# Performance work log

Measured on AMD Instinct MI355X. Metric: run time of the kernel, lower is better.

The kernel has to match this reference:

```python
import jax, jax.numpy as jnp
import numpy as np

DIM, INNER, NH = 256, 64, 8
HD = INNER // NH  # 8
B, H, W = 2, 48, 48
EPS = 1e-6


def _ln2d(x, w, b):
    # channel-first LayerNorm over dim=1, biased variance (matches LayerNorm2d)
    u = x.mean(axis=1, keepdims=True)
    s = ((x - u) ** 2).mean(axis=1, keepdims=True)
    xn = (x - u) / jnp.sqrt(s + EPS)
    return w[None, :, None, None] * xn + b[None, :, None, None]


def _conv1x1(x, w, b):
    return jnp.einsum('oc,bchw->bohw', w, x) + b[None, :, None, None]


def _attn(q, k, v):
    # q,k,v: [B, INNER, H, W] -> global attention over HW tokens per head
    Bq, C, Hh, Ww = q.shape
    split = lambda t: t.reshape(Bq, NH, HD, Hh * Ww)
    q, k, v = split(q), split(k), split(v)
    scale = HD ** -0.5
    attn = jnp.einsum('bhdn,bhdm->bhnm', q, k) * scale  # [B,nh,HW,HW]
    attn = jax.nn.softmax(attn, axis=-1)
    out = jnp.einsum('bhnm,bhdm->bhdn', attn, v)
    return out.reshape(Bq, C, Hh, Ww)


def setup_inputs() -> dict:
    key = jax.random.key(0)
    ks = jax.random.split(key, 12)
    w = lambda k, o, i: jax.random.normal(k, (o, i), dtype=jnp.float32) * 0.02
    d = {
        'f_rgb': jax.random.normal(ks[0], (B, DIM, H, W), dtype=jnp.float32),
        'f_ir': jax.random.normal(ks[1], (B, DIM, H, W), dtype=jnp.float32),
        'nr_w': jnp.ones(DIM), 'nr_b': jnp.zeros(DIM),
        'ni_w': jnp.ones(DIM), 'ni_b': jnp.zeros(DIM),
        'qr_w': w(ks[2], INNER, DIM), 'qr_b': jnp.zeros(INNER),
        'kvi_w': w(ks[3], 2 * INNER, DIM), 'kvi_b': jnp.zeros(2 * INNER),
        'qi_w': w(ks[4], INNER, DIM), 'qi_b': jnp.zeros(INNER),
        'kvr_w': w(ks[5], 2 * INNER, DIM), 'kvr_b': jnp.zeros(2 * INNER),
        'pr_w': w(ks[6], DIM, INNER), 'pr_b': jnp.zeros(DIM),
        'pr_lnw': jnp.ones(DIM), 'pr_lnb': jnp.zeros(DIM),
        'pi_w': w(ks[7], DIM, INNER), 'pi_b': jnp.zeros(DIM),
        'pi_lnw': jnp.ones(DIM), 'pi_lnb': jnp.zeros(DIM),
        'gr_w': w(ks[8], DIM, 2 * DIM), 'gr_b': jnp.zeros(DIM),
        'gi_w': w(ks[9], DIM, 2 * DIM), 'gi_b': jnp.zeros(DIM),
    }
    return d


def reference(f_rgb, f_ir, nr_w, nr_b, ni_w, ni_b, qr_w, qr_b, kvi_w, kvi_b,
              qi_w, qi_b, kvr_w, kvr_b, pr_w, pr_b, pr_lnw, pr_lnb,
              pi_w, pi_b, pi_lnw, pi_lnb, gr_w, gr_b, gi_w, gi_b):
    n_rgb = _ln2d(f_rgb, nr_w, nr_b)
    n_ir = _ln2d(f_ir, ni_w, ni_b)

    # RGB queries attend to IR keys/values
    q_r = _conv1x1(n_rgb, qr_w, qr_b)
    kv_i = _conv1x1(n_ir, kvi_w, kvi_b)
    k_i, v_i = kv_i[:, :INNER], kv_i[:, INNER:]
    rgb_cross = _attn(q_r, k_i, v_i)
    rgb_cross = _ln2d(_conv1x1(rgb_cross, pr_w, pr_b), pr_lnw, pr_lnb)
    gate_r = jax.nn.sigmoid(_conv1x1(jnp.concatenate([f_rgb, rgb_cross], axis=1), gr_w, gr_b))
    f_rgb_out = f_rgb + gate_r * rgb_cross

    # IR queries attend to RGB keys/values
    q_i = _conv1x1(n_ir, qi_w, qi_b)
    kv_r = _conv1x1(n_rgb, kvr_w, kvr_b)
    k_r, v_r = kv_r[:, :INNER], kv_r[:, INNER:]
    ir_cross = _attn(q_i, k_r, v_r)
    ir_cross = _ln2d(_conv1x1(ir_cross, pi_w, pi_b), pi_lnw, pi_lnb)
    gate_i = jax.nn.sigmoid(_conv1x1(jnp.concatenate([f_ir, ir_cross], axis=1), gi_w, gi_b))
    f_ir_out = f_ir + gate_i * ir_cross

    return (f_rgb_out, f_ir_out)
```

## Files before the change

kernel.cpp:

```cpp
#include <hip/hip_runtime.h>

static constexpr int kDim   = 256;
static constexpr int kInner = 64;
static constexpr int kNH    = 8;
static constexpr int kB     = 2;
static constexpr int kP     = 2304;
static constexpr float kScaleL2 = 0.5100697891920077f;
static constexpr float kEps   = 1e-6f;

typedef __fp16   fp16x2 __attribute__((ext_vector_type(2)));
typedef _Float16 half4f __attribute__((ext_vector_type(4)));
typedef _Float16 half8  __attribute__((ext_vector_type(8)));
typedef float    f32x4  __attribute__((ext_vector_type(4)));

static constexpr size_t oXq  = 0;
static constexpr size_t oQ16 = 2359296;
static constexpr size_t oK16 = 2949120;
static constexpr size_t oV16 = 3538944;
static constexpr size_t oA16 = 4128768;
static constexpr size_t oW16 = 7077888;
static constexpr size_t kInpStride = 294912;

__global__ __launch_bounds__(256) void prep(
    const float* __restrict__ x0, const float* __restrict__ w0,
    const float* __restrict__ b0, const float* __restrict__ x1,
    const float* __restrict__ w1, const float* __restrict__ b1,
    _Float16* __restrict__ Xq,
    const float* __restrict__ qr_w, const float* __restrict__ kvr_w,
    const float* __restrict__ qi_w, const float* __restrict__ kvi_w,
    const float* __restrict__ pr_w, const float* __restrict__ pi_w,
    const float* __restrict__ gr_w, const float* __restrict__ gi_w,
    _Float16* __restrict__ w16)
{
    if (blockIdx.x >= 576) {
        const int flat = blockIdx.x - 576;
        const int y = flat >> 6, x = flat & 63;
        const float* src; _Float16* dst; int n;
        _Float16* Aq = w16;
        _Float16* Ap = w16 + 98304;
        _Float16* Ag = w16 + 131072;
        switch (y) {
            case 0: src = qr_w;  dst = Aq;          n = 16384;  break;
            case 1: src = kvr_w; dst = Aq + 16384;  n = 32768;  break;
            case 2: src = qi_w;  dst = Aq + 49152;  n = 16384;  break;
            case 3: src = kvi_w; dst = Aq + 65536;  n = 32768;  break;
            case 4: src = pr_w;  dst = Ap;          n = 16384;  break;
            case 5: src = pi_w;  dst = Ap + 16384;  n = 16384;  break;
            case 6: src = gr_w;  dst = Ag;          n = 131072; break;
            default:src = gi_w;  dst = Ag + 131072; n = 131072; break;
        }
        for (int i = x * 256 + threadIdx.x; i < n; i += 64 * 256)
            dst[i] = (_Float16)src[i];
        return;
    }
    __shared__ float sb[16][16];
    __shared__ float ssb[16][16];
    const int fid = blockIdx.x;
    const int xcd = fid & 7, q = fid >> 3;
    const int inp = (xcd >> 2) & 1, bb = (xcd >> 1) & 1, half = xcd & 1;
    const float* x = inp ? x1 : x0;
    const float* w = inp ? w1 : w0;
    const float* b = inp ? b1 : b0;
    const int pos = threadIdx.x & 15;
    const int grp = threadIdx.x >> 4;
    const int p   = half * 1152 + q * 16 + pos;
    const size_t base = (size_t)bb * kDim * kP + p;
    const int c0 = grp * 16;

    float v[16];
    float s = 0.f, ss = 0.f;
    #pragma unroll
    for (int j = 0; j < 16; ++j) {
        v[j] = x[base + (size_t)(c0 + j) * kP];
        s += v[j]; ss += v[j] * v[j];
    }
    sb[grp][pos] = s; ssb[grp][pos] = ss;
    __syncthreads();
    float st = 0.f, sst = 0.f;
    #pragma unroll
    for (int g = 0; g < 16; ++g) { st += sb[g][pos]; sst += ssb[g][pos]; }
    const float mean = st * (1.f / kDim);
    const float rstd = rsqrtf(sst * (1.f / kDim) - mean * mean + kEps);
    half8 h0, h1;
    #pragma unroll
    for (int j = 0; j < 8; ++j) {
        h0[j] = (_Float16)((v[j]     - mean) * rstd * w[c0 + j]     + b[c0 + j]);
        h1[j] = (_Float16)((v[j + 8] - mean) * rstd * w[c0 + j + 8] + b[c0 + j + 8]);
    }
    _Float16* dst = Xq + ((size_t)(inp * 2 + bb) * kP + p) * 256 + c0;
    *(half8*)dst       = h0;
    *(half8*)(dst + 8) = h1;
}

template <int M, int K, int EPI>
__global__ __launch_bounds__(256) void gemm_f16(
    const _Float16* __restrict__ A,
    const _Float16* __restrict__ B,
    const float* __restrict__ b0, const float* __restrict__ b1,
    const float* __restrict__ b2, const float* __restrict__ b3,
    _Float16* __restrict__ o16a, _Float16* __restrict__ o16b, _Float16* __restrict__ o16c,
    const float* __restrict__ f0, const float* __restrict__ f1,
    float* __restrict__ outp)
{
    constexpr int MT64 = M / 64;
    const int fid = blockIdx.x;
    const int xcd = fid & 7, q = fid >> 3;
    const int s = (xcd >> 2) & 1, bb = (xcd >> 1) & 1, half = xcd & 1;
    const int ot64 = (q % MT64) * 64;
    const int pt   = q / MT64;
    const int wv = threadIdx.x >> 6, lane = threadIdx.x & 63;
    const int r16 = lane & 15, g = lane >> 4;
    const int ot = ot64 + wv * 16;
    const int p0 = half * 1152 + pt * 64;
    const int combo = s * 2 + bb;

    const _Float16* Ar = A + ((size_t)s * M + ot + r16) * K + 8 * g;
    const _Float16* Br = B + ((size_t)combo * kP + p0 + r16) * K + 8 * g;
    f32x4 acc0[4], acc1[4];
    #pragma unroll
    for (int ps = 0; ps < 4; ++ps) {
        acc0[ps] = (f32x4){0.f, 0.f, 0.f, 0.f};
        acc1[ps] = (f32x4){0.f, 0.f, 0.f, 0.f};
    }
    #pragma unroll 4
    for (int c0 = 0; c0 < K; c0 += 32) {
        const half8 a8 = *(const half8*)(Ar + c0);
        half8 b8[4];
        #pragma unroll
        for (int ps = 0; ps < 4; ++ps)
            b8[ps] = *(const half8*)(Br + (size_t)(16 * ps) * K + c0);
        const half4f al = {a8[0], a8[1], a8[2], a8[3]};
        const half4f ah = {a8[4], a8[5], a8[6], a8[7]};
        #pragma unroll
        for (int ps = 0; ps < 4; ++ps) {
            const half4f bl = {b8[ps][0], b8[ps][1], b8[ps][2], b8[ps][3]};
            const half4f bh = {b8[ps][4], b8[ps][5], b8[ps][6], b8[ps][7]};
            acc0[ps] = __builtin_amdgcn_mfma_f32_16x16x16f16(al, bl, acc0[ps], 0, 0, 0);
            acc1[ps] = __builtin_amdgcn_mfma_f32_16x16x16f16(ah, bh, acc1[ps], 0, 0, 0);
        }
    }
    const int obase = ot + 4 * g;

    #pragma unroll
    for (int ps = 0; ps < 4; ++ps) {
        float acc[4];
        #pragma unroll
        for (int i = 0; i < 4; ++i) acc[i] = acc0[ps][i] + acc1[ps][i];
        const int p = p0 + 16 * ps + r16;

        if constexpr (EPI == 0) {
            const int dlo = 4 * (g & 1);
            if (ot < 64) {
                const float* qb = s ? b1 : b0;
                const float4 bv = *(const float4*)(qb + obase);
                const int h = (ot >> 3) + (g >> 1);
                half4f o = { (_Float16)((acc[0] + bv.x) * kScaleL2), (_Float16)((acc[1] + bv.y) * kScaleL2),
                             (_Float16)((acc[2] + bv.z) * kScaleL2), (_Float16)((acc[3] + bv.w) * kScaleL2) };
                *(half4f*)(o16a + (((size_t)combo * 8 + h) * kP + p) * 8 + dlo) = o;
            } else if (ot < 128) {
                const float* kb = s ? b3 : b2;
                const float4 bv = *(const float4*)(kb + obase - 64);
                const int h = ((ot - 64) >> 3) + (g >> 1);
                half4f o = { (_Float16)(acc[0] + bv.x), (_Float16)(acc[1] + bv.y),
                             (_Float16)(acc[2] + bv.z), (_Float16)(acc[3] + bv.w) };
                *(half4f*)(o16b + (((size_t)combo * 8 + h) * kP + p) * 8 + dlo) = o;
            } else {
                const float* kb = s ? b3 : b2;
                const float4 bv = *(const float4*)(kb + obase - 64);
                const int h = ((ot - 128) >> 3) + (g >> 1);
                const float* bvp = (const float*)&bv;
                #pragma unroll
                for (int i = 0; i < 4; ++i)
                    o16c[(((size_t)combo * 8 + h) * 8 + dlo + i) * kP + p] = (_Float16)(acc[i] + bvp[i]);
            }
        } else {
            const float* gb = s ? b1 : b0;
            const float4 bv = *(const float4*)(gb + obase);
            const float* bvp = (const float*)&bv;
            const half4f cx = *(const half4f*)(B + ((size_t)combo * kP + p) * 512 + 256 + obase);
            const float* F = s ? f1 : f0;
            #pragma unroll
            for (int i = 0; i < 4; ++i) {
                const int o = obase + i;
                const float gt = 1.f / (1.f + __expf(-(acc[i] + bvp[i])));
                const float fb = F[((size_t)bb * kDim + o) * kP + p];
                outp[((size_t)combo * kDim + o) * kP + p] = fb + gt * (float)cx[i];
            }
        }
    }
}

__global__ __launch_bounds__(256) void proj_ln(
    const _Float16* __restrict__ a16, const _Float16* __restrict__ Ap,
    const float* __restrict__ pb0, const float* __restrict__ pb1,
    const float* __restrict__ w0, const float* __restrict__ b0,
    const float* __restrict__ w1, const float* __restrict__ b1,
    const float* __restrict__ f0, const float* __restrict__ f1,
    _Float16* __restrict__ Xg)
{
    __shared__ float sb[4][4][16];
    __shared__ float ssb[4][4][16];
    const int fid = blockIdx.x;
    const int xcd = fid & 7, q = fid >> 3;
    const int s = (xcd >> 2) & 1, bb = (xcd >> 1) & 1, half = xcd & 1;
    const int wv = threadIdx.x >> 6, lane = threadIdx.x & 63;
    const int r16 = lane & 15, g = lane >> 4;
    const int p = half * 1152 + q * 16 + r16;
    const int combo = s * 2 + bb;
    const float* pb = s ? pb1 : pb0;
    const float* w  = s ? w1 : w0;
    const float* b  = s ? b1 : b0;
    const float* F  = s ? f1 : f0;

    const _Float16* Br = a16 + ((size_t)combo * kP + p) * 64 + 8 * g;
    const half8 bA = *(const half8*)Br;
    const half8 bB = *(const half8*)(Br + 32);
    const half4f bl0 = {bA[0], bA[1], bA[2], bA[3]};
    const half4f bh0 = {bA[4], bA[5], bA[6], bA[7]};
    const half4f bl1 = {bB[0], bB[1], bB[2], bB[3]};
    const half4f bh1 = {bB[4], bB[5], bB[6], bB[7]};

    float cval[4][4];
    float psum = 0.f, psq = 0.f;
    #pragma unroll
    for (int t = 0; t < 4; ++t) {
        const int ot = wv * 64 + t * 16;
        const _Float16* Ar = Ap + ((size_t)s * 256 + ot + r16) * 64 + 8 * g;
        const half8 aA = *(const half8*)Ar;
        const half8 aB = *(const half8*)(Ar + 32);
        const half4f al0 = {aA[0], aA[1], aA[2], aA[3]};
        const half4f ah0 = {aA[4], aA[5], aA[6], aA[7]};
        const half4f al1 = {aB[0], aB[1], aB[2], aB[3]};
        const half4f ah1 = {aB[4], aB[5], aB[6], aB[7]};
        f32x4 acc0 = __builtin_amdgcn_mfma_f32_16x16x16f16(al0, bl0, (f32x4){0.f,0.f,0.f,0.f}, 0, 0, 0);
        acc0 = __builtin_amdgcn_mfma_f32_16x16x16f16(al1, bl1, acc0, 0, 0, 0);
        f32x4 acc1 = __builtin_amdgcn_mfma_f32_16x16x16f16(ah0, bh0, (f32x4){0.f,0.f,0.f,0.f}, 0, 0, 0);
        acc1 = __builtin_amdgcn_mfma_f32_16x16x16f16(ah1, bh1, acc1, 0, 0, 0);
        const float4 bv = *(const float4*)(pb + ot + 4 * g);
        const float* bvp = (const float*)&bv;
        #pragma unroll
        for (int i = 0; i < 4; ++i) {
            const float v = acc0[i] + acc1[i] + bvp[i];
            cval[t][i] = v;
            psum += v; psq += v * v;
        }
    }
    sb[wv][g][r16] = psum; ssb[wv][g][r16] = psq;
    __syncthreads();
    float st = 0.f, sst = 0.f;
    #pragma unroll
    for (int w2 = 0; w2 < 4; ++w2)
        #pragma unroll
        for (int g2 = 0; g2 < 4; ++g2) { st += sb[w2][g2][r16]; sst += ssb[w2][g2][r16]; }
    const float mean = st * (1.f / kDim);
    const float rstd = rsqrtf(sst * (1.f / kDim) - mean * mean + kEps);

    _Float16* xrow = Xg + ((size_t)combo * kP + p) * 512;
    #pragma unroll
    for (int t = 0; t < 4; ++t) {
        const int o4 = wv * 64 + t * 16 + 4 * g;
        const float4 lw = *(const float4*)(w + o4);
        const float4 lb = *(const float4*)(b + o4);
        const float* lwp = (const float*)&lw;
        const float* lbp = (const float*)&lb;
        half4f o;
        #pragma unroll
        for (int i = 0; i < 4; ++i)
            o[i] = (_Float16)((cval[t][i] - mean) * rstd * lwp[i] + lbp[i]);
        *(half4f*)(xrow + 256 + o4) = o;
        half4f r;
        #pragma unroll
        for (int i = 0; i < 4; ++i)
            r[i] = (_Float16)F[((size_t)bb * kDim + o4 + i) * kP + p];
        *(half4f*)(xrow + o4) = r;
    }
}

__global__ __launch_bounds__(256) void attn_mfma(
    const _Float16* __restrict__ q16, const _Float16* __restrict__ k16,
    const _Float16* __restrict__ vt16, _Float16* __restrict__ a16)
{
    __shared__ _Float16 Ksm[16 * 64 * 4];
    __shared__ _Float16 Vsm[16 * 66 * 4];
    const int st = blockIdx.z;
    const _Float16* Qg = q16  + (size_t)st * kInpStride;
    const _Float16* Kg = k16  + (size_t)(1 - st) * kInpStride;
    const _Float16* Vg = vt16 + (size_t)(1 - st) * kInpStride;
    const int bh = blockIdx.y;
    const int bb = bh >> 3, h = bh & 7;
    const int tid  = threadIdx.x;
    const int wv   = tid >> 6;
    const int lane = tid & 63;
    const int r16  = lane & 15;
    const int g    = lane >> 4;

    #pragma unroll
    for (int j = 0; j < 2; ++j) {
        const int s = tid + 256 * j;
        const int kt = s >> 5, m = s & 31;
        *(half4f*)(Ksm + (kt * 64 + 32 + m) * 4) = (half4f){0, 0, 0, 0};
        const int rv = 8 + (m & 7), gv = m >> 3;
        const half4f vv = (rv == 8)
            ? (half4f){(_Float16)1.f, (_Float16)1.f, (_Float16)1.f, (_Float16)1.f}
            : (half4f){0, 0, 0, 0};
        *(half4f*)(Vsm + (kt * 66 + gv * 16 + rv) * 4) = vv;
    }

    const int qg = blockIdx.x * 64 + wv * 16 + r16;
    half4f qf = (half4f){0, 0, 0, 0};
    if (g < 2) qf = *(const half4f*)(Qg + ((size_t)bh * kP + qg) * 8 + g * 4);

    const int vd = tid >> 5, vc8 = (tid & 31) * 8;
    const int vkt = vc8 >> 4, vgv = (vc8 & 15) >> 2;
    _Float16* kdst = Ksm + ((tid >> 4) * 64 + (tid & 15)) * 4;
    _Float16* vdst = Vsm + (vkt * 66 + vgv * 16 + vd) * 4;
    const _Float16* ksrc = Kg + ((size_t)bh * kP + tid) * 8;
    const _Float16* vsrc = Vg + (size_t)(bh * 8 + vd) * kP + vc8;

    half8 kreg = *(const half8*)ksrc;
    half8 vreg = *(const half8*)vsrc;

    f32x4 of0 = (f32x4){0.f, 0.f, 0.f, 0.f};
    f32x4 of1 = (f32x4){0.f, 0.f, 0.f, 0.f};

    for (int ch = 0; ch < 9; ++ch) {
        if (ch) __syncthreads();
        *(half4f*)kdst        = (half4f){kreg[0], kreg[1], kreg[2], kreg[3]};
        *(half4f*)(kdst + 64) = (half4f){kreg[4], kreg[5], kreg[6], kreg[7]};
        *(half4f*)vdst        = (half4f){vreg[0], vreg[1], vreg[2], vreg[3]};
        *(half4f*)(vdst + 64) = (half4f){vreg[4], vreg[5], vreg[6], vreg[7]};
        __syncthreads();
        if (ch < 8) {
            kreg = *(const half8*)(ksrc + (size_t)(ch + 1) * 2048);
            vreg = *(const half8*)(vsrc + (size_t)(ch + 1) * 256);
        }
        #pragma unroll
        for (int kt = 0; kt < 16; ++kt) {
            const half4f kf = *(const half4f*)(Ksm + (kt * 64 + lane) * 4);
            f32x4 sv = __builtin_amdgcn_mfma_f32_16x16x16f16(kf, qf, (f32x4){0.f,0.f,0.f,0.f}, 0, 0, 0);
            const float e0 = __builtin_amdgcn_exp2f(sv[0]);
            const float e1 = __builtin_amdgcn_exp2f(sv[1]);
            const float e2 = __builtin_amdgcn_exp2f(sv[2]);
            const float e3 = __builtin_amdgcn_exp2f(sv[3]);
            const fp16x2 lo = __builtin_amdgcn_cvt_pkrtz(e0, e1);
            const fp16x2 hi = __builtin_amdgcn_cvt_pkrtz(e2, e3);
            const half4f pf = { (_Float16)lo[0], (_Float16)lo[1],
                                (_Float16)hi[0], (_Float16)hi[1] };
            const half4f vf = *(const half4f*)(Vsm + (kt * 66 + lane) * 4);
            if (kt & 1) of1 = __builtin_amdgcn_mfma_f32_16x16x16f16(vf, pf, of1, 0, 0, 0);
            else        of0 = __builtin_amdgcn_mfma_f32_16x16x16f16(vf, pf, of0, 0, 0, 0);
        }
    }
    const f32x4 of = of0 + of1;
    const float rsv = __shfl(of[0], 32 + r16, 64);
    const float inv = 1.f / rsv;
    if (g < 2) {
        half4f o = { (_Float16)(of[0] * inv), (_Float16)(of[1] * inv),
                     (_Float16)(of[2] * inv), (_Float16)(of[3] * inv) };
        *(half4f*)(a16 + ((size_t)(st * 2 + bb) * kP + qg) * 64 + h * 8 + g * 4) = o;
    }
}

extern "C" void kernel_launch(void* const* d_in, const int* in_sizes, int n_in,
                              void* d_out, int out_size, void* d_ws, size_t ws_size,
                              hipStream_t stream)
{
    const float* f_rgb  = (const float*)d_in[0];
    const float* f_ir   = (const float*)d_in[1];
    const float* nr_w   = (const float*)d_in[2];
    const float* nr_b   = (const float*)d_in[3];
    const float* ni_w   = (const float*)d_in[4];
    const float* ni_b   = (const float*)d_in[5];
    const float* qr_w   = (const float*)d_in[6];
    const float* qr_b   = (const float*)d_in[7];
    const float* kvi_w  = (const float*)d_in[8];
    const float* kvi_b  = (const float*)d_in[9];
    const float* qi_w   = (const float*)d_in[10];
    const float* qi_b   = (const float*)d_in[11];
    const float* kvr_w  = (const float*)d_in[12];
    const float* kvr_b  = (const float*)d_in[13];
    const float* pr_w   = (const float*)d_in[14];
    const float* pr_b   = (const float*)d_in[15];
    const float* pr_lnw = (const float*)d_in[16];
    const float* pr_lnb = (const float*)d_in[17];
    const float* pi_w   = (const float*)d_in[18];
    const float* pi_b   = (const float*)d_in[19];
    const float* pi_lnw = (const float*)d_in[20];
    const float* pi_lnb = (const float*)d_in[21];
    const float* gr_w   = (const float*)d_in[22];
    const float* gr_b   = (const float*)d_in[23];
    const float* gi_w   = (const float*)d_in[24];
    const float* gi_b   = (const float*)d_in[25];

    _Float16* hb   = (_Float16*)d_ws;
    _Float16* Xq   = hb + oXq;
    _Float16* q16  = hb + oQ16;
    _Float16* k16  = hb + oK16;
    _Float16* vt16 = hb + oV16;
    _Float16* a16  = hb + oA16;
    _Float16* Xg   = hb;
    _Float16* W16  = hb + oW16;
    _Float16* Aq   = W16;
    _Float16* Ap   = W16 + 98304;
    _Float16* Ag   = W16 + 131072;

    float* outp = (float*)d_out;
    const dim3 blk(256);

    prep<<<dim3(1088), blk, 0, stream>>>(f_rgb, nr_w, nr_b, f_ir, ni_w, ni_b, Xq,
                                         qr_w, kvr_w, qi_w, kvi_w, pr_w, pi_w, gr_w, gi_w, W16);
    gemm_f16<192, 256, 0><<<dim3(432), blk, 0, stream>>>(
        Aq, Xq, qr_b, qi_b, kvr_b, kvi_b, q16, k16, vt16, nullptr, nullptr, nullptr);
    attn_mfma<<<dim3(36, 16, 2), blk, 0, stream>>>(q16, k16, vt16, a16);
    proj_ln<<<dim3(576), blk, 0, stream>>>(a16, Ap, pr_b, pi_b,
                                           pr_lnw, pr_lnb, pi_lnw, pi_lnb,
                                           f_rgb, f_ir, Xg);
    gemm_f16<256, 512, 2><<<dim3(576), blk, 0, stream>>>(
        Ag, Xg, gr_b, gi_b, nullptr, nullptr, nullptr, nullptr, nullptr, f_rgb, f_ir, outp);
}
```

Before: 98.66 us.

## Load K/V fragments directly from global memory in attention, dropping LDS staging

The attention kernel no longer stages K and V tiles through shared memory with block-wide barriers. Each lane now loads its own MFMA operand fragment straight from global memory (relying on cache) and synthesizes the zero padding and the ones row used for the row-sum inline. This removes LDS writes, LDS reads and syncthreads per chunk. In exchange, the four waves in a block each issue redundant, small, strided global loads, and the load latency is no longer explicitly prefetched.

```diff
diff --git a/kernel.cpp b/kernel.cpp
--- a/kernel.cpp
+++ b/kernel.cpp
@@ -280,8 +280,6 @@
     const _Float16* __restrict__ q16, const _Float16* __restrict__ k16,
     const _Float16* __restrict__ vt16, _Float16* __restrict__ a16)
 {
-    __shared__ _Float16 Ksm[16 * 64 * 4];
-    __shared__ _Float16 Vsm[16 * 66 * 4];
     const int st = blockIdx.z;
     const _Float16* Qg = q16  + (size_t)st * kInpStride;
     const _Float16* Kg = k16  + (size_t)(1 - st) * kInpStride;
@@ -294,62 +292,38 @@
     const int r16  = lane & 15;
     const int g    = lane >> 4;
 
-    #pragma unroll
-    for (int j = 0; j < 2; ++j) {
-        const int s = tid + 256 * j;
-        const int kt = s >> 5, m = s & 31;
-        *(half4f*)(Ksm + (kt * 64 + 32 + m) * 4) = (half4f){0, 0, 0, 0};
-        const int rv = 8 + (m & 7), gv = m >> 3;
-        const half4f vv = (rv == 8)
-            ? (half4f){(_Float16)1.f, (_Float16)1.f, (_Float16)1.f, (_Float16)1.f}
-            : (half4f){0, 0, 0, 0};
-        *(half4f*)(Vsm + (kt * 66 + gv * 16 + rv) * 4) = vv;
-    }
-
     const int qg = blockIdx.x * 64 + wv * 16 + r16;
     half4f qf = (half4f){0, 0, 0, 0};
     if (g < 2) qf = *(const half4f*)(Qg + ((size_t)bh * kP + qg) * 8 + g * 4);
 
-    const int vd = tid >> 5, vc8 = (tid & 31) * 8;
-    const int vkt = vc8 >> 4, vgv = (vc8 & 15) >> 2;
-    _Float16* kdst = Ksm + ((tid >> 4) * 64 + (tid & 15)) * 4;
-    _Float16* vdst = Vsm + (vkt * 66 + vgv * 16 + vd) * 4;
-    const _Float16* ksrc = Kg + ((size_t)bh * kP + tid) * 8;
-    const _Float16* vsrc = Vg + (size_t)(bh * 8 + vd) * kP + vc8;
-
-    half8 kreg = *(const half8*)ksrc;
-    half8 vreg = *(const half8*)vsrc;
+    const bool kact = (g < 2);
+    const bool vact = (r16 < 8);
+    const bool vone = (r16 == 8);
+    const _Float16* kptr = Kg + ((size_t)bh * kP + r16) * 8 + (g & 1) * 4;
+    const _Float16* vptr = Vg + (size_t)(bh * 8 + (r16 & 7)) * kP + 4 * g;
+    const half4f vones = {(_Float16)1.f, (_Float16)1.f, (_Float16)1.f, (_Float16)1.f};
 
     f32x4 of0 = (f32x4){0.f, 0.f, 0.f, 0.f};
     f32x4 of1 = (f32x4){0.f, 0.f, 0.f, 0.f};
 
-    for (int ch = 0; ch < 9; ++ch) {
-        if (ch) __syncthreads();
-        *(half4f*)kdst        = (half4f){kreg[0], kreg[1], kreg[2], kreg[3]};
-        *(half4f*)(kdst + 64) = (half4f){kreg[4], kreg[5], kreg[6], kreg[7]};
-        *(half4f*)vdst        = (half4f){vreg[0], vreg[1], vreg[2], vreg[3]};
-        *(half4f*)(vdst + 64) = (half4f){vreg[4], vreg[5], vreg[6], vreg[7]};
-        __syncthreads();
-        if (ch < 8) {
-            kreg = *(const half8*)(ksrc + (size_t)(ch + 1) * 2048);
-            vreg = *(const half8*)(vsrc + (size_t)(ch + 1) * 256);
-        }
-        #pragma unroll
-        for (int kt = 0; kt < 16; ++kt) {
-            const half4f kf = *(const half4f*)(Ksm + (kt * 64 + lane) * 4);
-            f32x4 sv = __builtin_amdgcn_mfma_f32_16x16x16f16(kf, qf, (f32x4){0.f,0.f,0.f,0.f}, 0, 0, 0);
-            const float e0 = __builtin_amdgcn_exp2f(sv[0]);
-            const float e1 = __builtin_amdgcn_exp2f(sv[1]);
-            const float e2 = __builtin_amdgcn_exp2f(sv[2]);
-            const float e3 = __builtin_amdgcn_exp2f(sv[3]);
-            const fp16x2 lo = __builtin_amdgcn_cvt_pkrtz(e0, e1);
-            const fp16x2 hi = __builtin_amdgcn_cvt_pkrtz(e2, e3);
-            const half4f pf = { (_Float16)lo[0], (_Float16)lo[1],
-                                (_Float16)hi[0], (_Float16)hi[1] };
-            const half4f vf = *(const half4f*)(Vsm + (kt * 66 + lane) * 4);
-            if (kt & 1) of1 = __builtin_amdgcn_mfma_f32_16x16x16f16(vf, pf, of1, 0, 0, 0);
-            else        of0 = __builtin_amdgcn_mfma_f32_16x16x16f16(vf, pf, of0, 0, 0, 0);
-        }
+    #pragma unroll 4
+    for (int kt = 0; kt < 144; ++kt) {
+        half4f kf = (half4f){0, 0, 0, 0};
+        if (kact) kf = *(const half4f*)(kptr + (size_t)kt * 128);
+        half4f vf = (half4f){0, 0, 0, 0};
+        if (vact) vf = *(const half4f*)(vptr + (size_t)kt * 16);
+        if (vone) vf = vones;
+        f32x4 sv = __builtin_amdgcn_mfma_f32_16x16x16f16(kf, qf, (f32x4){0.f,0.f,0.f,0.f}, 0, 0, 0);
+        const float e0 = __builtin_amdgcn_exp2f(sv[0]);
+        const float e1 = __builtin_amdgcn_exp2f(sv[1]);
+        const float e2 = __builtin_amdgcn_exp2f(sv[2]);
+        const float e3 = __builtin_amdgcn_exp2f(sv[3]);
+        const fp16x2 lo = __builtin_amdgcn_cvt_pkrtz(e0, e1);
+        const fp16x2 hi = __builtin_amdgcn_cvt_pkrtz(e2, e3);
+        const half4f pf = { (_Float16)lo[0], (_Float16)lo[1],
+                            (_Float16)hi[0], (_Float16)hi[1] };
+        if (kt & 1) of1 = __builtin_amdgcn_mfma_f32_16x16x16f16(vf, pf, of1, 0, 0, 0);
+        else        of0 = __builtin_amdgcn_mfma_f32_16x16x16f16(vf, pf, of0, 0, 0, 0);
     }
     const f32x4 of = of0 + of1;
     const float rsv = __shfl(of[0], 32 + r16, 64);
```

Result: slower. 143.9 us (+45.8%).
